# Performance work log

Measured on AMD Instinct MI355X. Metric: run time of the kernel, lower is better.

The kernel has to match this reference:

```python
import jax, jax.numpy as jnp
import numpy as np

N, D, H = 8192, 64, 256

def setup_inputs() -> dict:
    key = jax.random.key(0)
    k0, k1, k2, k3, k4 = jax.random.split(key, 5)
    y = jax.random.normal(k0, (N, D), jnp.float32)
    t = jax.random.uniform(k1, (1,), jnp.float32)
    # diffeq MLP params (time-conditioned 1-hidden-layer tanh net)
    W1 = jax.random.normal(k2, (D, H), jnp.float32) / np.float32(np.sqrt(D))
    b1 = jnp.zeros((H,), jnp.float32)
    wt = jax.random.normal(k3, (H,), jnp.float32) * jnp.float32(0.1)
    W2 = jax.random.normal(k4, (H, D), jnp.float32) / np.float32(np.sqrt(H))
    b2 = jnp.zeros((D,), jnp.float32)
    return {"t": t, "y": y, "W1": W1, "b1": b1, "wt": wt, "W2": W2, "b2": b2}

def reference(t, y, W1, b1, wt, W2, b2):
    ts = t[0]

    def f_single(yi):  # yi: [D] -> dy_i: [D]
        h = jnp.tanh(yi @ W1 + ts * wt + b1)
        return h @ W2 + b2

    # dy = diffeq(t, y): batched forward pass
    h = jnp.tanh(y @ W1 + ts * wt + b1)          # [N, H]
    dy = h @ W2 + b2                              # [N, D]

    # brute-force divergence = trace of per-sample Jacobian d(dy_i)/d(y_i)
    # (replaces the O(D) looped torch.autograd.grad calls with one batched
    #  forward-mode Jacobian computation)
    div = jax.vmap(lambda yi: jnp.trace(jax.jacfwd(f_single)(yi)))(y)  # [N]

    # original returns (dy, -divergence.view(N,1)); concatenated for a single output
    return jnp.concatenate([dy, -div[:, None]], axis=1)  # [N, D+1]
```

## Files before the change

kernel.cpp:

```cpp
#include <hip/hip_runtime.h>

#define NROWS 8192
#define DDIM 64
#define HDIM 256
#define HPAD 264

using bf16x8 = __attribute__((ext_vector_type(8))) short;
using f32x4  = __attribute__((ext_vector_type(4))) float;

__device__ __forceinline__ unsigned short f2bf(float x) {
    unsigned u = __float_as_uint(x);
    u += 0x7FFFu + ((u >> 16) & 1u);
    return (unsigned short)(u >> 16);
}

__device__ __forceinline__ float fast_tanh(float x) {
    float e = __expf(2.0f * x);
    return 1.0f - 2.0f * __builtin_amdgcn_rcpf(e + 1.0f);
}

__global__ void prep_kernel(const float* __restrict__ t,
                            const float* __restrict__ W1,
                            const float* __restrict__ b1,
                            const float* __restrict__ wt,
                            const float* __restrict__ W2,
                            unsigned short* __restrict__ W1t,
                            unsigned short* __restrict__ W2t,
                            float* __restrict__ Cb,
                            float* __restrict__ Sv) {
    int gid = blockIdx.x * 256 + threadIdx.x;
    if (blockIdx.x < 64) {
        int m = gid >> 6, k = gid & 63;
        W1t[gid] = f2bf(W1[k * HDIM + m]);
    } else if (blockIdx.x < 128) {
        int i = gid - 16384;
        int n = i >> 8, k = i & 255;
        W2t[i] = f2bf(W2[k * DDIM + n]);
    } else {
        int m = threadIdx.x;
        Cb[m] = b1[m] + t[0] * wt[m];
        float s = 0.f;
        #pragma unroll
        for (int k = 0; k < DDIM; ++k) s += W1[k * HDIM + m] * W2[m * DDIM + k];
        Sv[m] = s;
    }
}

__global__ __launch_bounds__(256)
void ode_main(const float* __restrict__ y,
              const unsigned short* __restrict__ W1t,
              const unsigned short* __restrict__ W2t,
              const float* __restrict__ Cb,
              const float* __restrict__ Sv,
              const float* __restrict__ b2,
              float* __restrict__ out) {
    const int tid  = threadIdx.x;
    const int w    = tid >> 6;
    const int lane = tid & 63;
    const int l16  = lane & 15;
    const int quad = lane >> 4;
    const int row0 = blockIdx.x * 16;

    __shared__ __align__(16) unsigned short h_lds[16 * HPAD];
    __shared__ float dvp[64];

    bf16x8 afr[2];
    const float* yrow = y + (size_t)(row0 + l16) * DDIM;
    #pragma unroll
    for (int ks = 0; ks < 2; ++ks) {
        const float4 f0 = *(const float4*)(yrow + ks * 32 + quad * 8);
        const float4 f1 = *(const float4*)(yrow + ks * 32 + quad * 8 + 4);
        bf16x8 a;
        a[0] = (short)f2bf(f0.x); a[1] = (short)f2bf(f0.y);
        a[2] = (short)f2bf(f0.z); a[3] = (short)f2bf(f0.w);
        a[4] = (short)f2bf(f1.x); a[5] = (short)f2bf(f1.y);
        a[6] = (short)f2bf(f1.z); a[7] = (short)f2bf(f1.w);
        afr[ks] = a;
    }

    f32x4 acc[4];
    #pragma unroll
    for (int ct = 0; ct < 4; ++ct) acc[ct] = (f32x4){0.f, 0.f, 0.f, 0.f};

    #pragma unroll
    for (int ct = 0; ct < 4; ++ct) {
        const int m = w * 64 + ct * 16 + l16;
        #pragma unroll
        for (int ks = 0; ks < 2; ++ks) {
            bf16x8 b = *(const bf16x8*)(W1t + m * DDIM + ks * 32 + quad * 8);
            acc[ct] = __builtin_amdgcn_mfma_f32_16x16x32_bf16(afr[ks], b, acc[ct], 0, 0, 0);
        }
    }

    float dv[4] = {0.f, 0.f, 0.f, 0.f};
    #pragma unroll
    for (int ct = 0; ct < 4; ++ct) {
        const int m = w * 64 + ct * 16 + l16;
        const float cb = Cb[m];
        const float sv = Sv[m];
        #pragma unroll
        for (int r = 0; r < 4; ++r) {
            float z = acc[ct][r] + cb;
            float h = fast_tanh(z);
            dv[r] += (1.f - h * h) * sv;
            h_lds[(quad * 4 + r) * HPAD + m] = f2bf(h);
        }
    }
    #pragma unroll
    for (int off = 8; off; off >>= 1) {
        #pragma unroll
        for (int r = 0; r < 4; ++r) dv[r] += __shfl_down(dv[r], off, 16);
    }
    if (l16 == 0) {
        #pragma unroll
        for (int r = 0; r < 4; ++r) dvp[w * 16 + quad * 4 + r] = dv[r];
    }
    __syncthreads();

    f32x4 acc2 = (f32x4){0.f, 0.f, 0.f, 0.f};
    const int n = w * 16 + l16;
    #pragma unroll
    for (int ks = 0; ks < 8; ++ks) {
        bf16x8 a = *(const bf16x8*)(&h_lds[l16 * HPAD + ks * 32 + quad * 8]);
        bf16x8 b = *(const bf16x8*)(W2t + n * HDIM + ks * 32 + quad * 8);
        acc2 = __builtin_amdgcn_mfma_f32_16x16x32_bf16(a, b, acc2, 0, 0, 0);
    }
    const float b2v = b2[n];
    #pragma unroll
    for (int r = 0; r < 4; ++r) {
        const int row = quad * 4 + r;
        out[(size_t)(row0 + row) * (DDIM + 1) + n] = acc2[r] + b2v;
    }

    if (w == 0 && lane < 16) {
        float s = dvp[lane] + dvp[16 + lane] + dvp[32 + lane] + dvp[48 + lane];
        out[(size_t)(row0 + lane) * (DDIM + 1) + DDIM] = -s;
    }
}

extern "C" void kernel_launch(void* const* d_in, const int* in_sizes, int n_in,
                              void* d_out, int out_size, void* d_ws, size_t ws_size,
                              hipStream_t stream) {
    const float* t  = (const float*)d_in[0];
    const float* y  = (const float*)d_in[1];
    const float* W1 = (const float*)d_in[2];
    const float* b1 = (const float*)d_in[3];
    const float* wt = (const float*)d_in[4];
    const float* W2 = (const float*)d_in[5];
    const float* b2 = (const float*)d_in[6];
    float* out = (float*)d_out;

    unsigned short* W1t = (unsigned short*)d_ws;
    unsigned short* W2t = (unsigned short*)((char*)d_ws + 32768);
    float* Cb = (float*)((char*)d_ws + 65536);
    float* Sv = (float*)((char*)d_ws + 66560);

    prep_kernel<<<129, 256, 0, stream>>>(t, W1, b1, wt, W2, W1t, W2t, Cb, Sv);
    ode_main<<<NROWS / 16, 256, 0, stream>>>(y, W1t, W2t, Cb, Sv, b2, out);
}
```

Measured before the change: 75.33 us.

## Fuse weight prep into main kernel, staging bf16 weights in shared memory

Removes the separate prep kernel. Each block now loads W1 and W2 from global fp32, converts them to bf16 into padded LDS tiles, and recomputes the per-hidden divergence scale and the time-conditioned bias locally. This eliminates one launch and the workspace round trip. In exchange, every block redundantly reads and converts all weights and recomputes the strided dot products. It also uses a large LDS footprint and scalar strided LDS gathers for the MFMA B fragments.

```diff
diff --git a/kernel.cpp b/kernel.cpp
--- a/kernel.cpp
+++ b/kernel.cpp
@@ -3,6 +3,8 @@
 #define NROWS 8192
 #define DDIM 64
 #define HDIM 256
+#define W1S 260
+#define W2S 68
 #define HPAD 264
 
 using bf16x8 = __attribute__((ext_vector_type(8))) short;
@@ -13,47 +15,23 @@
     u += 0x7FFFu + ((u >> 16) & 1u);
     return (unsigned short)(u >> 16);
 }
-
+__device__ __forceinline__ unsigned pack2(float a, float b) {
+    return (unsigned)f2bf(a) | ((unsigned)f2bf(b) << 16);
+}
 __device__ __forceinline__ float fast_tanh(float x) {
     float e = __expf(2.0f * x);
     return 1.0f - 2.0f * __builtin_amdgcn_rcpf(e + 1.0f);
 }
 
-__global__ void prep_kernel(const float* __restrict__ t,
-                            const float* __restrict__ W1,
-                            const float* __restrict__ b1,
-                            const float* __restrict__ wt,
-                            const float* __restrict__ W2,
-                            unsigned short* __restrict__ W1t,
-                            unsigned short* __restrict__ W2t,
-                            float* __restrict__ Cb,
-                            float* __restrict__ Sv) {
-    int gid = blockIdx.x * 256 + threadIdx.x;
-    if (blockIdx.x < 64) {
-        int m = gid >> 6, k = gid & 63;
-        W1t[gid] = f2bf(W1[k * HDIM + m]);
-    } else if (blockIdx.x < 128) {
-        int i = gid - 16384;
-        int n = i >> 8, k = i & 255;
-        W2t[i] = f2bf(W2[k * DDIM + n]);
-    } else {
-        int m = threadIdx.x;
-        Cb[m] = b1[m] + t[0] * wt[m];
-        float s = 0.f;
-        #pragma unroll
-        for (int k = 0; k < DDIM; ++k) s += W1[k * HDIM + m] * W2[m * DDIM + k];
-        Sv[m] = s;
-    }
-}
-
 __global__ __launch_bounds__(256)
-void ode_main(const float* __restrict__ y,
-              const unsigned short* __restrict__ W1t,
-              const unsigned short* __restrict__ W2t,
-              const float* __restrict__ Cb,
-              const float* __restrict__ Sv,
-              const float* __restrict__ b2,
-              float* __restrict__ out) {
+void ode_fused(const float* __restrict__ t,
+               const float* __restrict__ y,
+               const float* __restrict__ W1,
+               const float* __restrict__ b1,
+               const float* __restrict__ wt,
+               const float* __restrict__ W2,
+               const float* __restrict__ b2,
+               float* __restrict__ out) {
     const int tid  = threadIdx.x;
     const int w    = tid >> 6;
     const int lane = tid & 63;
@@ -61,33 +39,71 @@
     const int quad = lane >> 4;
     const int row0 = blockIdx.x * 16;
 
+    __shared__ __align__(16) unsigned short w1s[64 * W1S];
+    __shared__ __align__(16) unsigned short w2s[256 * W2S];
     __shared__ __align__(16) unsigned short h_lds[16 * HPAD];
+    __shared__ float svs[HDIM];
     __shared__ float dvp[64];
+
+    const float4* W1v = (const float4*)W1;
+    const float4* W2v = (const float4*)W2;
+    #pragma unroll
+    for (int i = 0; i < 16; ++i) {
+        float4 f = W1v[i * 256 + tid];
+        int p = (i * 256 + tid) * 4;
+        unsigned* dst = (unsigned*)&w1s[(p >> 8) * W1S + (p & 255)];
+        dst[0] = pack2(f.x, f.y); dst[1] = pack2(f.z, f.w);
+    }
+    #pragma unroll
+    for (int i = 0; i < 16; ++i) {
+        float4 f = W2v[i * 256 + tid];
+        int p = (i * 256 + tid) * 4;
+        unsigned* dst = (unsigned*)&w2s[(p >> 6) * W2S + (p & 63)];
+        dst[0] = pack2(f.x, f.y); dst[1] = pack2(f.z, f.w);
+    }
+    {
+        float s = 0.f;
+        #pragma unroll
+        for (int k = 0; k < DDIM; ++k) s += W1[k * HDIM + tid] * W2[tid * DDIM + k];
+        svs[tid] = s;
+    }
 
     bf16x8 afr[2];
     const float* yrow = y + (size_t)(row0 + l16) * DDIM;
     #pragma unroll
     for (int ks = 0; ks < 2; ++ks) {
-        const float4 f0 = *(const float4*)(yrow + ks * 32 + quad * 8);
-        const float4 f1 = *(const float4*)(yrow + ks * 32 + quad * 8 + 4);
+        float4 f0 = *(const float4*)(yrow + ks * 32 + quad * 8);
+        float4 f1 = *(const float4*)(yrow + ks * 32 + quad * 8 + 4);
         bf16x8 a;
-        a[0] = (short)f2bf(f0.x); a[1] = (short)f2bf(f0.y);
-        a[2] = (short)f2bf(f0.z); a[3] = (short)f2bf(f0.w);
-        a[4] = (short)f2bf(f1.x); a[5] = (short)f2bf(f1.y);
-        a[6] = (short)f2bf(f1.z); a[7] = (short)f2bf(f1.w);
+        a[0]=(short)f2bf(f0.x); a[1]=(short)f2bf(f0.y); a[2]=(short)f2bf(f0.z); a[3]=(short)f2bf(f0.w);
+        a[4]=(short)f2bf(f1.x); a[5]=(short)f2bf(f1.y); a[6]=(short)f2bf(f1.z); a[7]=(short)f2bf(f1.w);
         afr[ks] = a;
     }
+
+    const float ts = t[0];
+    float cbv[4];
+    #pragma unroll
+    for (int ct = 0; ct < 4; ++ct) {
+        int m = w * 64 + ct * 16 + l16;
+        cbv[ct] = b1[m] + ts * wt[m];
+    }
+    const int ncol = w * 16 + l16;
+    const float b2v = b2[ncol];
+
+    __syncthreads();
 
     f32x4 acc[4];
     #pragma unroll
     for (int ct = 0; ct < 4; ++ct) acc[ct] = (f32x4){0.f, 0.f, 0.f, 0.f};
-
     #pragma unroll
     for (int ct = 0; ct < 4; ++ct) {
         const int m = w * 64 + ct * 16 + l16;
         #pragma unroll
         for (int ks = 0; ks < 2; ++ks) {
-            bf16x8 b = *(const bf16x8*)(W1t + m * DDIM + ks * 32 + quad * 8);
+            bf16x8 b;
+            #pragma unroll
+            for (int j = 0; j < 8; ++j)
+                b[j] = (short)w1s[(ks * 32 + quad * 8 + j) * W1S + m];
             acc[ct] = __builtin_amdgcn_mfma_f32_16x16x32_bf16(afr[ks], b, acc[ct], 0, 0, 0);
         }
     }
@@ -96,11 +112,10 @@
     #pragma unroll
     for (int ct = 0; ct < 4; ++ct) {
         const int m = w * 64 + ct * 16 + l16;
-        const float cb = Cb[m];
-        const float sv = Sv[m];
+        const float sv = svs[m];
         #pragma unroll
         for (int r = 0; r < 4; ++r) {
-            float z = acc[ct][r] + cb;
+            float z = acc[ct][r] + cbv[ct];
             float h = fast_tanh(z);
             dv[r] += (1.f - h * h) * sv;
             h_lds[(quad * 4 + r) * HPAD + m] = f2bf(h);
@@ -118,18 +133,19 @@
     __syncthreads();
 
     f32x4 acc2 = (f32x4){0.f, 0.f, 0.f, 0.f};
-    const int n = w * 16 + l16;
     #pragma unroll
     for (int ks = 0; ks < 8; ++ks) {
         bf16x8 a = *(const bf16x8*)(&h_lds[l16 * HPAD + ks * 32 + quad * 8]);
-        bf16x8 b = *(const bf16x8*)(W2t + n * HDIM + ks * 32 + quad * 8);
+        bf16x8 b;
+        #pragma unroll
+        for (int j = 0; j < 8; ++j)
+            b[j] = (short)w2s[(ks * 32 + quad * 8 + j) * W2S + ncol];
         acc2 = __builtin_amdgcn_mfma_f32_16x16x32_bf16(a, b, acc2, 0, 0, 0);
     }
-    const float b2v = b2[n];
     #pragma unroll
     for (int r = 0; r < 4; ++r) {
         const int row = quad * 4 + r;
-        out[(size_t)(row0 + row) * (DDIM + 1) + n] = acc2[r] + b2v;
+        out[(size_t)(row0 + row) * (DDIM + 1) + ncol] = acc2[r] + b2v;
     }
 
     if (w == 0 && lane < 16) {
@@ -150,11 +166,5 @@
     const float* b2 = (const float*)d_in[6];
     float* out = (float*)d_out;
 
-    unsigned short* W1t = (unsigned short*)d_ws;
-    unsigned short* W2t = (unsigned short*)((char*)d_ws + 32768);
-    float* Cb = (float*)((char*)d_ws + 65536);
-    float* Sv = (float*)((char*)d_ws + 66560);
-
-    prep_kernel<<<129, 256, 0, stream>>>(t, W1, b1, wt, W2, W1t, W2t, Cb, Sv);
-    ode_main<<<NROWS / 16, 256, 0, stream>>>(y, W1t, W2t, Cb, Sv, b2, out);
+    ode_fused<<<NROWS / 16, 256, 0, stream>>>(t, y, W1, b1, wt, W2, b2, out);
 }
```

After: 75.76 us. No clear change (+0.6%).
